# Performance work log

Measured on AMD Instinct MI355X. Metric: run time of the kernel, lower is better.

## Reference

```python
import jax, jax.numpy as jnp
import numpy as np

N = 50000   # nodes
E = 100000  # directed edges
G = 2048    # graphs in batch
D = 32      # hidden dim
F_NODE = 11
F_EDGE = 4


def setup_inputs() -> dict:
    key = jax.random.key(0)
    ks = jax.random.split(key, 12)
    s = 0.1
    return {
        "x": jax.random.normal(ks[0], (N, F_NODE), dtype=jnp.float32),
        "edge_attr": jax.random.uniform(ks[1], (E, F_EDGE), dtype=jnp.float32),
        "lin0_w": jax.random.normal(ks[2], (D, F_NODE), dtype=jnp.float32) * s,
        "lin0_b": jnp.zeros((D,), jnp.float32),
        "nn_w": jax.random.normal(ks[3], (D * D, F_EDGE), dtype=jnp.float32) * s,
        "nn_b": jnp.zeros((D * D,), jnp.float32),
        "root_w": jax.random.normal(ks[4], (D, D), dtype=jnp.float32) * s,
        "conv_b": jnp.zeros((D,), jnp.float32),
        "gru_wi": jax.random.normal(ks[5], (3 * D, D), dtype=jnp.float32) * s,
        "gru_wh": jax.random.normal(ks[6], (3 * D, D), dtype=jnp.float32) * s,
        "gru_bi": jnp.zeros((3 * D,), jnp.float32),
        "gru_bh": jnp.zeros((3 * D,), jnp.float32),
        "lin1_w": jax.random.normal(ks[7], (2, D), dtype=jnp.float32) * s,
        "lin1_b": jnp.zeros((2,), jnp.float32),
        "edge_index": jax.random.randint(ks[8], (2, E), 0, N, dtype=jnp.int32),
        "batch": jnp.sort(jax.random.randint(ks[9], (N,), 0, G, dtype=jnp.int32)),
    }


def _gru_step(m, h, wi, wh, bi, bh):
    # single-step torch.nn.GRU cell math
    gi = m @ wi.T + bi            # [N, 3D]
    gh = h @ wh.T + bh            # [N, 3D]
    ir, iz, inn = jnp.split(gi, 3, axis=-1)
    hr, hz, hn = jnp.split(gh, 3, axis=-1)
    r = jax.nn.sigmoid(ir + hr)
    z = jax.nn.sigmoid(iz + hz)
    n = jnp.tanh(inn + r * hn)
    return (1.0 - z) * n + z * h


def reference(x, edge_attr, lin0_w, lin0_b, nn_w, nn_b, root_w, conv_b,
              gru_wi, gru_wh, gru_bi, gru_bh, lin1_w, lin1_b,
              edge_index, batch):
    src, dst = edge_index[0], edge_index[1]
    out = jax.nn.relu(x @ lin0_w.T + lin0_b)   # [N, D]
    h = out
    # per-edge 32x32 weight from edge MLP (edge_attr fixed -> hoisted out of loop)
    W_e = (edge_attr @ nn_w.T + nn_b).reshape(E, D, D)
    for _ in range(3):
        msg = jnp.einsum('ei,eio->eo', out[src], W_e)                  # [E, D]
        aggr = jax.ops.segment_sum(msg, dst, num_segments=N)           # add-aggregate
        m = jax.nn.relu(aggr + out @ root_w + conv_b)                  # NNConv root + bias
        h = _gru_step(m, h, gru_wi, gru_wh, gru_bi, gru_bh)
        out = h
    cnt = jax.ops.segment_sum(jnp.ones((N,), x.dtype), batch, num_segments=G)
    pooled = jax.ops.segment_sum(out, batch, num_segments=G) / jnp.maximum(cnt, 1.0)[:, None]
    logits = pooled @ lin1_w.T + lin1_b                                # [G, 2]
    return jax.nn.log_softmax(logits, axis=1)
```

## Files before the change

kernel.cpp:

```cpp
#include <hip/hip_runtime.h>
#include <hip/hip_bf16.h>

#define NN 50000
#define EE 100000
#define GG 2048
#define NB2 391

__device__ __forceinline__ float b2f(unsigned short u) {
    union { unsigned int i; float f; } x; x.i = (unsigned int)u << 16; return x.f;
}
__device__ __forceinline__ unsigned short f2b(float f) {
    union { float f; unsigned int i; } x; x.f = f;
    unsigned int b = x.i + (0x7FFFu + ((x.i >> 16) & 1u));
    return (unsigned short)(b >> 16);
}

__global__ void k_init(const float* __restrict__ x, const float* __restrict__ w,
                       const float* __restrict__ b, float* __restrict__ feat) {
    int idx = blockIdx.x * blockDim.x + threadIdx.x;
    if (idx >= NN * 32) return;
    int n = idx >> 5, o = idx & 31;
    const float* xr = x + n * 11;
    const float* wr = w + o * 11;
    float acc = b[o];
#pragma unroll
    for (int i = 0; i < 11; ++i) acc += xr[i] * wr[i];
    feat[idx] = fmaxf(acc, 0.f);
}

__global__ void k_prep(const float* __restrict__ nnw, const float* __restrict__ nnb,
                       const float* __restrict__ wi, const float* __restrict__ wh,
                       float* __restrict__ Wre, float* __restrict__ WyT,
                       float* __restrict__ wiT, float* __restrict__ whT) {
    int idx = blockIdx.x * blockDim.x + threadIdx.x;
    if (idx < 5120) {
        int c = idx >> 5, i = idx & 31;
        float v;
        if (c < 128) v = nnw[((i << 5) + (c & 31)) * 4 + (c >> 5)];
        else         v = nnb[(i << 5) + (c - 128)];
        Wre[idx] = v;
    } else if (idx < 10240) {
        int j = idx - 5120;
        int i = j / 160, c = j - i * 160;
        float v;
        if (c < 128) v = nnw[((i << 5) + (c & 31)) * 4 + (c >> 5)];
        else         v = nnb[(i << 5) + (c - 128)];
        WyT[j] = v;
    } else if (idx < 13312) {
        int j = idx - 10240;
        int k = j / 96, c = j - k * 96;
        wiT[j] = wi[c * 32 + k];
    } else if (idx < 16384) {
        int j = idx - 13312;
        int k = j / 96, c = j - k * 96;
        whT[j] = wh[c * 32 + k];
    }
}

__global__ void k_hist(const int* __restrict__ ei, int* __restrict__ cnt) {
    int e = blockIdx.x * blockDim.x + threadIdx.x;
    if (e >= EE) return;
    atomicAdd(&cnt[ei[EE + e]], 1);
    atomicAdd(&cnt[NN + ei[e]], 1);
}

__global__ __launch_bounds__(256) void k_scan1(const int* __restrict__ cnt,
                                               int* __restrict__ tmp,
                                               int* __restrict__ bsum) {
    __shared__ int sd[256];
    int t = threadIdx.x;
    int i = blockIdx.x * 256 + t;
    int v = (i < 2 * NN) ? cnt[i] : 0;
    sd[t] = v;
    __syncthreads();
#pragma unroll
    for (int off = 1; off < 256; off <<= 1) {
        int x = (t >= off) ? sd[t - off] : 0;
        __syncthreads();
        sd[t] += x;
        __syncthreads();
    }
    if (i < 2 * NN) tmp[i] = sd[t];
    if (t == 255) bsum[blockIdx.x] = sd[255];
}

__global__ __launch_bounds__(512) void k_scan2(int* __restrict__ bsum) {
    __shared__ int sd[512];
    int t = threadIdx.x;
    int v = (t < NB2) ? bsum[t] : 0;
    sd[t] = v;
    __syncthreads();
#pragma unroll
    for (int off = 1; off < 512; off <<= 1) {
        int x = (t >= off) ? sd[t - off] : 0;
        __syncthreads();
        sd[t] += x;
        __syncthreads();
    }
    if (t < NB2) bsum[t] = sd[t];
}

__global__ void k_scan3(const int* __restrict__ cnt, const int* __restrict__ tmp,
                        const int* __restrict__ bsum, int* __restrict__ row_ptr,
                        int* __restrict__ cursor, int* __restrict__ out_ptr,
                        int* __restrict__ cursor2) {
    int i = blockIdx.x * blockDim.x + threadIdx.x;
    if (i >= 2 * NN) return;
    int base = (blockIdx.x > 0) ? bsum[blockIdx.x - 1] : 0;
    int excl = base + tmp[i] - cnt[i];
    if (i < NN) {
        row_ptr[i] = excl;
        cursor[i] = excl;
        if (i == 0) row_ptr[NN] = EE;
    } else {
        int j = i - NN;
        out_ptr[j] = excl - EE;
        cursor2[j] = excl - EE;
        if (j == 0) out_ptr[NN] = EE;
    }
}

__global__ void k_scatter(const int* __restrict__ ei, const float* __restrict__ ea,
                          int* __restrict__ cursor, int* __restrict__ cursor2,
                          int* __restrict__ esrc, float4* __restrict__ eea,
                          int* __restrict__ oslot, float4* __restrict__ oea) {
    int e = blockIdx.x * blockDim.x + threadIdx.x;
    if (e >= EE) return;
    int s = ei[e], d = ei[EE + e];
    float4 a = make_float4(ea[e * 4 + 0], ea[e * 4 + 1], ea[e * 4 + 2], ea[e * 4 + 3]);
    int slot = atomicAdd(&cursor[d], 1);
    esrc[slot] = s;
    eea[slot] = a;
    int pos = atomicAdd(&cursor2[s], 1);
    oslot[pos] = slot;
    oea[pos] = a;
}

__global__ __launch_bounds__(256) void k_y(const float* __restrict__ feat,
                                           const float* __restrict__ Wre,
                                           unsigned short* __restrict__ yb) {
    int lane = threadIdx.x & 63;
    int wv = __builtin_amdgcn_readfirstlane(threadIdx.x >> 6);
    int n = blockIdx.x * 64 + lane;
    if (n >= NN) return;
    int c0 = blockIdx.y * 40 + wv * 10;
    float fr[32];
    const float4* f4 = (const float4*)(feat + (long)n * 32);
#pragma unroll
    for (int q = 0; q < 8; ++q) {
        float4 v = f4[q];
        fr[4 * q + 0] = v.x; fr[4 * q + 1] = v.y;
        fr[4 * q + 2] = v.z; fr[4 * q + 3] = v.w;
    }
    float acc[10];
#pragma unroll
    for (int cc = 0; cc < 10; ++cc) {
        const float* w = Wre + (c0 + cc) * 32;
        float a = 0.f;
#pragma unroll
        for (int i = 0; i < 32; ++i) a += fr[i] * w[i];
        acc[cc] = a;
    }
    unsigned short* yr = yb + (long)n * 160 + c0;
#pragma unroll
    for (int q = 0; q < 5; ++q) {
        unsigned int wlo = f2b(acc[2 * q]);
        unsigned int whi = f2b(acc[2 * q + 1]);
        ((unsigned int*)yr)[q] = wlo | (whi << 16);
    }
}

__global__ __launch_bounds__(256) void k_msg(
    const unsigned short* __restrict__ yb, const int* __restrict__ esrc,
    const float4* __restrict__ eea, float* __restrict__ msg) {
    int idx = blockIdx.x * 256 + threadIdx.x;
    if (idx >= EE * 32) return;
    int slot = idx >> 5, o = idx & 31;
    int s = esrc[slot];
    float4 a = eea[slot];
    const unsigned short* yr = yb + (long)s * 160;
    float y0 = b2f(yr[o]);
    float y1 = b2f(yr[32 + o]);
    float y2 = b2f(yr[64 + o]);
    float y3 = b2f(yr[96 + o]);
    float y4 = b2f(yr[128 + o]);
    msg[idx] = y4 + a.x * y0 + a.y * y1 + a.z * y2 + a.w * y3;
}

__global__ __launch_bounds__(256) void k_conv_update(
    const float* __restrict__ msg_in, const int* __restrict__ row_ptr,
    const float* __restrict__ rootw, const float* __restrict__ convb,
    const float* __restrict__ wiT, const float* __restrict__ whT,
    const float* __restrict__ bi, const float* __restrict__ bh,
    const float* __restrict__ WyT, const int* __restrict__ out_ptr,
    const int* __restrict__ oslot, const float4* __restrict__ oea,
    float* __restrict__ feat, float* __restrict__ msg_out, int write_msg) {
    __shared__ float fs[32][32];
    __shared__ float ms[32][32];
    int t = threadIdx.x;
    int g = t >> 5, o = t & 31;
    int nb = blockIdx.x * 32 + g * 4;
    float f[4], m[4];
#pragma unroll
    for (int j = 0; j < 4; ++j) {
        int n = nb + j;
        bool v = (n < NN);
        f[j] = v ? feat[(long)n * 32 + o] : 0.f;
        fs[g * 4 + j][o] = f[j];
        m[j] = convb[o];
        if (v) {
            int e0 = row_ptr[n], e1 = row_ptr[n + 1];
            for (int e = e0; e < e1; ++e)
                m[j] += msg_in[((long)e << 5) + o];
        }
    }
    __syncthreads();
#pragma unroll 4
    for (int i = 0; i < 32; ++i) {
        float rw = rootw[i * 32 + o];
#pragma unroll
        for (int j = 0; j < 4; ++j) m[j] += fs[g * 4 + j][i] * rw;
    }
#pragma unroll
    for (int j = 0; j < 4; ++j) {
        m[j] = fmaxf(m[j], 0.f);
        ms[g * 4 + j][o] = m[j];
    }
    __syncthreads();
    float bir = bi[o], biz = bi[32 + o], bin_ = bi[64 + o];
    float bhr = bh[o], bhz = bh[32 + o], bhn = bh[64 + o];
    float gir[4], giz[4], gin_[4], ghr[4], ghz[4], ghn[4];
#pragma unroll
    for (int j = 0; j < 4; ++j) {
        gir[j] = bir; giz[j] = biz; gin_[j] = bin_;
        ghr[j] = bhr; ghz[j] = bhz; ghn[j] = bhn;
    }
#pragma unroll 2
    for (int k = 0; k < 32; ++k) {
        const float* wik = wiT + k * 96 + o;
        const float* whk = whT + k * 96 + o;
        float wir = wik[0], wiz = wik[32], win = wik[64];
        float whr = whk[0], whz = whk[32], whn = whk[64];
#pragma unroll
        for (int j = 0; j < 4; ++j) {
            float mk = ms[g * 4 + j][k], hk = fs[g * 4 + j][k];
            gir[j] += mk * wir;
            giz[j] += mk * wiz;
            gin_[j] += mk * win;
            ghr[j] += hk * whr;
            ghz[j] += hk * whz;
            ghn[j] += hk * whn;
        }
    }
    float fn[4];
#pragma unroll
    for (int j = 0; j < 4; ++j) {
        int n = nb + j;
        float r = 1.f / (1.f + __expf(-(gir[j] + ghr[j])));
        float z = 1.f / (1.f + __expf(-(giz[j] + ghz[j])));
        float nt = tanhf(gin_[j] + r * ghn[j]);
        fn[j] = (1.f - z) * nt + z * f[j];
        if (n < NN) feat[(long)n * 32 + o] = fn[j];
    }
    if (!write_msg) return;
#pragma unroll
    for (int j = 0; j < 4; ++j) fs[g * 4 + j][o] = fn[j];
    float ya[4][5];
#pragma unroll
    for (int j = 0; j < 4; ++j)
#pragma unroll
        for (int q = 0; q < 5; ++q) ya[j][q] = 0.f;
#pragma unroll 4
    for (int i = 0; i < 32; ++i) {
        const float* wy = WyT + i * 160 + o;
        float w0 = wy[0], w1 = wy[32], w2 = wy[64], w3 = wy[96], w4 = wy[128];
#pragma unroll
        for (int j = 0; j < 4; ++j) {
            float fv = fs[g * 4 + j][i];
            ya[j][0] += fv * w0;
            ya[j][1] += fv * w1;
            ya[j][2] += fv * w2;
            ya[j][3] += fv * w3;
            ya[j][4] += fv * w4;
        }
    }
#pragma unroll
    for (int j = 0; j < 4; ++j) {
        int n = nb + j;
        if (n < NN) {
            int p0 = out_ptr[n], p1 = out_ptr[n + 1];
            for (int p = p0; p < p1; ++p) {
                float4 a = oea[p];
                int slot = oslot[p];
                msg_out[((long)slot << 5) + o] =
                    ya[j][4] + a.x * ya[j][0] + a.y * ya[j][1]
                             + a.z * ya[j][2] + a.w * ya[j][3];
            }
        }
    }
}

__global__ __launch_bounds__(64) void k_pool_final(
    const float* __restrict__ feat, const int* __restrict__ batch,
    const float* __restrict__ w, const float* __restrict__ b,
    float* __restrict__ out) {
    int g = blockIdx.x;
    int t = threadIdx.x;
    int o = t & 31, h = t >> 5;
    int lo = 0, hi = NN;
    while (lo < hi) { int mid = (lo + hi) >> 1; if (batch[mid] < g) lo = mid + 1; else hi = mid; }
    int start = lo;
    hi = NN;
    while (lo < hi) { int mid = (lo + hi) >> 1; if (batch[mid] <= g) lo = mid + 1; else hi = mid; }
    int end = lo;
    float acc = 0.f;
    for (int n = start + h; n < end; n += 2) acc += feat[(long)n * 32 + o];
    acc += __shfl_xor(acc, 32, 64);
    float p = acc / fmaxf((float)(end - start), 1.f);
    float l0 = p * w[o], l1 = p * w[32 + o];
#pragma unroll
    for (int s = 16; s >= 1; s >>= 1) {
        l0 += __shfl_xor(l0, s, 64);
        l1 += __shfl_xor(l1, s, 64);
    }
    if (t == 0) {
        l0 += b[0]; l1 += b[1];
        float mx = fmaxf(l0, l1);
        float lse = mx + logf(__expf(l0 - mx) + __expf(l1 - mx));
        out[g * 2 + 0] = l0 - lse;
        out[g * 2 + 1] = l1 - lse;
    }
}

extern "C" void kernel_launch(void* const* d_in, const int* in_sizes, int n_in,
                              void* d_out, int out_size, void* d_ws, size_t ws_size,
                              hipStream_t stream) {
    const float* x        = (const float*)d_in[0];
    const float* edge_attr= (const float*)d_in[1];
    const float* lin0_w   = (const float*)d_in[2];
    const float* lin0_b   = (const float*)d_in[3];
    const float* nn_w     = (const float*)d_in[4];
    const float* nn_b     = (const float*)d_in[5];
    const float* root_w   = (const float*)d_in[6];
    const float* conv_b   = (const float*)d_in[7];
    const float* gru_wi   = (const float*)d_in[8];
    const float* gru_wh   = (const float*)d_in[9];
    const float* gru_bi   = (const float*)d_in[10];
    const float* gru_bh   = (const float*)d_in[11];
    const float* lin1_w   = (const float*)d_in[12];
    const float* lin1_b   = (const float*)d_in[13];
    const int*   edge_idx = (const int*)d_in[14];
    const int*   batch    = (const int*)d_in[15];
    float* out = (float*)d_out;

    float* ws     = (float*)d_ws;
    float* feat   = ws;
    float* Wre    = feat + (long)NN * 32;
    float* WyT    = Wre + 5120;
    float* wiT    = WyT + 5120;
    float* whT    = wiT + 3072;
    int*   cnt    = (int*)(whT + 3072);
    int*   tmp    = cnt + 2 * NN;
    int*   bsum   = tmp + 2 * NN;
    int*   row_ptr= bsum + 512;
    int*   cursor = row_ptr + NN + 1;
    int*   out_ptr= cursor + NN;
    int*   cursor2= out_ptr + NN + 1;
    int*   esrc   = cursor2 + NN;
    int*   oslot  = esrc + EE;
    size_t off = ((size_t)((char*)(oslot + EE) - (char*)d_ws) + 15) & ~(size_t)15;
    float4* eea  = (float4*)((char*)d_ws + off);
    float4* oea  = eea + EE;
    unsigned short* yb = (unsigned short*)(oea + EE);
    float* msgA  = (float*)(yb + (long)NN * 160);
    float* msgB  = msgA + (long)EE * 32;

    hipMemsetAsync(cnt, 0, 2 * NN * sizeof(int), stream);

    k_prep<<<64, 256, 0, stream>>>(nn_w, nn_b, gru_wi, gru_wh, Wre, WyT, wiT, whT);
    k_init<<<(NN * 32 + 255) / 256, 256, 0, stream>>>(x, lin0_w, lin0_b, feat);

    k_hist<<<(EE + 255) / 256, 256, 0, stream>>>(edge_idx, cnt);
    k_scan1<<<NB2, 256, 0, stream>>>(cnt, tmp, bsum);
    k_scan2<<<1, 512, 0, stream>>>(bsum);
    k_scan3<<<NB2, 256, 0, stream>>>(cnt, tmp, bsum, row_ptr, cursor, out_ptr, cursor2);
    k_scatter<<<(EE + 255) / 256, 256, 0, stream>>>(edge_idx, edge_attr, cursor, cursor2,
                                                    esrc, eea, oslot, oea);

    dim3 gy((NN + 63) / 64, 4);
    k_y<<<gy, 256, 0, stream>>>(feat, Wre, yb);
    k_msg<<<(EE * 32 + 255) / 256, 256, 0, stream>>>(yb, esrc, eea, msgA);

    k_conv_update<<<(NN + 31) / 32, 256, 0, stream>>>(msgA, row_ptr, root_w, conv_b,
                                                      wiT, whT, gru_bi, gru_bh, WyT,
                                                      out_ptr, oslot, oea,
                                                      feat, msgB, 1);
    k_conv_update<<<(NN + 31) / 32, 256, 0, stream>>>(msgB, row_ptr, root_w, conv_b,
                                                      wiT, whT, gru_bi, gru_bh, WyT,
                                                      out_ptr, oslot, oea,
                                                      feat, msgA, 1);
    k_conv_update<<<(NN + 31) / 32, 256, 0, stream>>>(msgA, row_ptr, root_w, conv_b,
                                                      wiT, whT, gru_bi, gru_bh, WyT,
                                                      out_ptr, oslot, oea,
                                                      feat, msgB, 0);

    k_pool_final<<<GG, 64, 0, stream>>>(feat, batch, lin1_w, lin1_b, out);
}
```

Measured before the change: 293.0 us.

## Merge setup kernels, fuse scatter with y, pack conv weights into float4 with packed FMA

Combines the init, prep and histogram kernels into one launch, and the scatter and y-projection kernels into another, to cut launch count and gaps. In the conv/GRU update kernel, the root and hidden-GRU weights are packed into one float4 table and the input-GRU weights into another. The root and hidden-gate matmuls now share one loop, shared memory is transposed and padded for float4 reads, and the arithmetic uses two-wide packed FMAs. The message projection now reads nn_w directly as float4, which removes the WyT transpose. The risks are higher register pressure and branch-divergent block roles inside the merged kernels.

```diff
diff --git a/kernel.cpp b/kernel.cpp
--- a/kernel.cpp
+++ b/kernel.cpp
@@ -6,6 +6,11 @@
 #define GG 2048
 #define NB2 391
 
+typedef float v2f __attribute__((ext_vector_type(2)));
+__device__ __forceinline__ v2f fma2(v2f a, float b, v2f c) {
+    return __builtin_elementwise_fma(a, (v2f){b, b}, c);
+}
+
 __device__ __forceinline__ float b2f(unsigned short u) {
     union { unsigned int i; float f; } x; x.i = (unsigned int)u << 16; return x.f;
 }
@@ -15,53 +20,51 @@
     return (unsigned short)(b >> 16);
 }
 
-__global__ void k_init(const float* __restrict__ x, const float* __restrict__ w,
-                       const float* __restrict__ b, float* __restrict__ feat) {
-    int idx = blockIdx.x * blockDim.x + threadIdx.x;
-    if (idx >= NN * 32) return;
-    int n = idx >> 5, o = idx & 31;
-    const float* xr = x + n * 11;
-    const float* wr = w + o * 11;
-    float acc = b[o];
-#pragma unroll
-    for (int i = 0; i < 11; ++i) acc += xr[i] * wr[i];
-    feat[idx] = fmaxf(acc, 0.f);
-}
-
-__global__ void k_prep(const float* __restrict__ nnw, const float* __restrict__ nnb,
-                       const float* __restrict__ wi, const float* __restrict__ wh,
-                       float* __restrict__ Wre, float* __restrict__ WyT,
-                       float* __restrict__ wiT, float* __restrict__ whT) {
-    int idx = blockIdx.x * blockDim.x + threadIdx.x;
-    if (idx < 5120) {
-        int c = idx >> 5, i = idx & 31;
-        float v;
-        if (c < 128) v = nnw[((i << 5) + (c & 31)) * 4 + (c >> 5)];
-        else         v = nnb[(i << 5) + (c - 128)];
-        Wre[idx] = v;
-    } else if (idx < 10240) {
-        int j = idx - 5120;
-        int i = j / 160, c = j - i * 160;
-        float v;
-        if (c < 128) v = nnw[((i << 5) + (c & 31)) * 4 + (c >> 5)];
-        else         v = nnb[(i << 5) + (c - 128)];
-        WyT[j] = v;
-    } else if (idx < 13312) {
-        int j = idx - 10240;
-        int k = j / 96, c = j - k * 96;
-        wiT[j] = wi[c * 32 + k];
-    } else if (idx < 16384) {
-        int j = idx - 13312;
-        int k = j / 96, c = j - k * 96;
-        whT[j] = wh[c * 32 + k];
-    }
-}
-
-__global__ void k_hist(const int* __restrict__ ei, int* __restrict__ cnt) {
-    int e = blockIdx.x * blockDim.x + threadIdx.x;
-    if (e >= EE) return;
-    atomicAdd(&cnt[ei[EE + e]], 1);
-    atomicAdd(&cnt[NN + ei[e]], 1);
+__global__ __launch_bounds__(256) void k_setup(
+    const float* __restrict__ x, const float* __restrict__ lw,
+    const float* __restrict__ lb, const float* __restrict__ nnw,
+    const float* __restrict__ nnb, const float* __restrict__ rootw,
+    const float* __restrict__ wi, const float* __restrict__ wh,
+    const int* __restrict__ ei, float* __restrict__ feat,
+    float* __restrict__ Wre, float4* __restrict__ rw4,
+    float4* __restrict__ wi4, int* __restrict__ cnt) {
+    int blk = blockIdx.x;
+    int t = threadIdx.x;
+    if (blk < 6250) {
+        int idx = blk * 256 + t;
+        if (idx >= NN * 32) return;
+        int n = idx >> 5, o = idx & 31;
+        const float* xr = x + n * 11;
+        const float* wr = lw + o * 11;
+        float acc = lb[o];
+#pragma unroll
+        for (int i = 0; i < 11; ++i) acc += xr[i] * wr[i];
+        feat[idx] = fmaxf(acc, 0.f);
+    } else if (blk < 6278) {
+        int idx = (blk - 6250) * 256 + t;
+        if (idx < 5120) {
+            int c = idx >> 5, i = idx & 31;
+            float v;
+            if (c < 128) v = nnw[((i << 5) + (c & 31)) * 4 + (c >> 5)];
+            else         v = nnb[(i << 5) + (c - 128)];
+            Wre[idx] = v;
+        } else if (idx < 6144) {
+            int j = idx - 5120;
+            int k = j >> 5, o = j & 31;
+            rw4[j] = make_float4(rootw[k * 32 + o], wh[o * 32 + k],
+                                 wh[(32 + o) * 32 + k], wh[(64 + o) * 32 + k]);
+        } else if (idx < 7168) {
+            int j = idx - 6144;
+            int k = j >> 5, o = j & 31;
+            wi4[j] = make_float4(wi[o * 32 + k], wi[(32 + o) * 32 + k],
+                                 wi[(64 + o) * 32 + k], 0.f);
+        }
+    } else {
+        int e = (blk - 6278) * 256 + t;
+        if (e >= EE) return;
+        atomicAdd(&cnt[ei[EE + e]], 1);
+        atomicAdd(&cnt[NN + ei[e]], 1);
+    }
 }
 
 __global__ __launch_bounds__(256) void k_scan1(const int* __restrict__ cnt,
@@ -120,37 +123,41 @@
     }
 }
 
-__global__ void k_scatter(const int* __restrict__ ei, const float* __restrict__ ea,
-                          int* __restrict__ cursor, int* __restrict__ cursor2,
-                          int* __restrict__ esrc, float4* __restrict__ eea,
-                          int* __restrict__ oslot, float4* __restrict__ oea) {
-    int e = blockIdx.x * blockDim.x + threadIdx.x;
-    if (e >= EE) return;
-    int s = ei[e], d = ei[EE + e];
-    float4 a = make_float4(ea[e * 4 + 0], ea[e * 4 + 1], ea[e * 4 + 2], ea[e * 4 + 3]);
-    int slot = atomicAdd(&cursor[d], 1);
-    esrc[slot] = s;
-    eea[slot] = a;
-    int pos = atomicAdd(&cursor2[s], 1);
-    oslot[pos] = slot;
-    oea[pos] = a;
-}
-
-__global__ __launch_bounds__(256) void k_y(const float* __restrict__ feat,
-                                           const float* __restrict__ Wre,
-                                           unsigned short* __restrict__ yb) {
+__global__ __launch_bounds__(256) void k_scatter_y(
+    const int* __restrict__ ei, const float* __restrict__ ea,
+    int* __restrict__ cursor, int* __restrict__ cursor2,
+    int* __restrict__ esrc, float4* __restrict__ eea,
+    int* __restrict__ oslot, float4* __restrict__ oea,
+    const float* __restrict__ feat, const float* __restrict__ Wre,
+    unsigned short* __restrict__ yb) {
+    int blk = blockIdx.x;
+    if (blk < 391) {
+        int e = blk * 256 + threadIdx.x;
+        if (e >= EE) return;
+        int s = ei[e], d = ei[EE + e];
+        float4 a = make_float4(ea[e * 4 + 0], ea[e * 4 + 1], ea[e * 4 + 2], ea[e * 4 + 3]);
+        int slot = atomicAdd(&cursor[d], 1);
+        esrc[slot] = s;
+        eea[slot] = a;
+        int pos = atomicAdd(&cursor2[s], 1);
+        oslot[pos] = slot;
+        oea[pos] = a;
+        return;
+    }
+    int by = blk - 391;
+    int bx = by % 782, q = by / 782;
     int lane = threadIdx.x & 63;
     int wv = __builtin_amdgcn_readfirstlane(threadIdx.x >> 6);
-    int n = blockIdx.x * 64 + lane;
+    int n = bx * 64 + lane;
     if (n >= NN) return;
-    int c0 = blockIdx.y * 40 + wv * 10;
+    int c0 = q * 40 + wv * 10;
     float fr[32];
     const float4* f4 = (const float4*)(feat + (long)n * 32);
 #pragma unroll
-    for (int q = 0; q < 8; ++q) {
-        float4 v = f4[q];
-        fr[4 * q + 0] = v.x; fr[4 * q + 1] = v.y;
-        fr[4 * q + 2] = v.z; fr[4 * q + 3] = v.w;
+    for (int qq = 0; qq < 8; ++qq) {
+        float4 v = f4[qq];
+        fr[4 * qq + 0] = v.x; fr[4 * qq + 1] = v.y;
+        fr[4 * qq + 2] = v.z; fr[4 * qq + 3] = v.w;
     }
     float acc[10];
 #pragma unroll
@@ -163,10 +170,10 @@
     }
     unsigned short* yr = yb + (long)n * 160 + c0;
 #pragma unroll
-    for (int q = 0; q < 5; ++q) {
-        unsigned int wlo = f2b(acc[2 * q]);
-        unsigned int whi = f2b(acc[2 * q + 1]);
-        ((unsigned int*)yr)[q] = wlo | (whi << 16);
+    for (int qq = 0; qq < 5; ++qq) {
+        unsigned int wlo = f2b(acc[2 * qq]);
+        unsigned int whi = f2b(acc[2 * qq + 1]);
+        ((unsigned int*)yr)[qq] = wlo | (whi << 16);
     }
 }
 
@@ -189,101 +196,109 @@
 
 __global__ __launch_bounds__(256) void k_conv_update(
     const float* __restrict__ msg_in, const int* __restrict__ row_ptr,
-    const float* __restrict__ rootw, const float* __restrict__ convb,
-    const float* __restrict__ wiT, const float* __restrict__ whT,
-    const float* __restrict__ bi, const float* __restrict__ bh,
-    const float* __restrict__ WyT, const int* __restrict__ out_ptr,
+    const float4* __restrict__ rw4, const float* __restrict__ convb,
+    const float4* __restrict__ wi4, const float* __restrict__ bi,
+    const float* __restrict__ bh, const float4* __restrict__ nnw4,
+    const float* __restrict__ nnb, const int* __restrict__ out_ptr,
     const int* __restrict__ oslot, const float4* __restrict__ oea,
     float* __restrict__ feat, float* __restrict__ msg_out, int write_msg) {
-    __shared__ float fs[32][32];
-    __shared__ float ms[32][32];
+    __shared__ float fsT[32][36];
+    __shared__ float msT[32][36];
     int t = threadIdx.x;
     int g = t >> 5, o = t & 31;
-    int nb = blockIdx.x * 32 + g * 4;
+    int gc = g * 4;
+    int nb = blockIdx.x * 32 + gc;
     float f[4], m[4];
+    float cb = convb[o];
 #pragma unroll
     for (int j = 0; j < 4; ++j) {
         int n = nb + j;
         bool v = (n < NN);
-        f[j] = v ? feat[(long)n * 32 + o] : 0.f;
-        fs[g * 4 + j][o] = f[j];
-        m[j] = convb[o];
+        f[j] = v ? feat[n * 32 + o] : 0.f;
+        m[j] = cb;
         if (v) {
             int e0 = row_ptr[n], e1 = row_ptr[n + 1];
             for (int e = e0; e < e1; ++e)
-                m[j] += msg_in[((long)e << 5) + o];
+                m[j] += msg_in[(e << 5) + o];
         }
     }
+    *(float4*)&fsT[o][gc] = make_float4(f[0], f[1], f[2], f[3]);
     __syncthreads();
+
+    float bhr = bh[o], bhz = bh[32 + o], bhn = bh[64 + o];
+    v2f m01 = {m[0], m[1]}, m23 = {m[2], m[3]};
+    v2f ghr01 = {bhr, bhr}, ghr23 = {bhr, bhr};
+    v2f ghz01 = {bhz, bhz}, ghz23 = {bhz, bhz};
+    v2f ghn01 = {bhn, bhn}, ghn23 = {bhn, bhn};
 #pragma unroll 4
     for (int i = 0; i < 32; ++i) {
-        float rw = rootw[i * 32 + o];
-#pragma unroll
-        for (int j = 0; j < 4; ++j) m[j] += fs[g * 4 + j][i] * rw;
-    }
-#pragma unroll
-    for (int j = 0; j < 4; ++j) {
-        m[j] = fmaxf(m[j], 0.f);
-        ms[g * 4 + j][o] = m[j];
-    }
+        float4 w = rw4[i * 32 + o];
+        float4 fv = *(const float4*)&fsT[i][gc];
+        v2f f01 = {fv.x, fv.y}, f23 = {fv.z, fv.w};
+        m01 = fma2(f01, w.x, m01);   m23 = fma2(f23, w.x, m23);
+        ghr01 = fma2(f01, w.y, ghr01); ghr23 = fma2(f23, w.y, ghr23);
+        ghz01 = fma2(f01, w.z, ghz01); ghz23 = fma2(f23, w.z, ghz23);
+        ghn01 = fma2(f01, w.w, ghn01); ghn23 = fma2(f23, w.w, ghn23);
+    }
+    float mm0 = fmaxf(m01.x, 0.f), mm1 = fmaxf(m01.y, 0.f);
+    float mm2 = fmaxf(m23.x, 0.f), mm3 = fmaxf(m23.y, 0.f);
+    *(float4*)&msT[o][gc] = make_float4(mm0, mm1, mm2, mm3);
     __syncthreads();
+
     float bir = bi[o], biz = bi[32 + o], bin_ = bi[64 + o];
-    float bhr = bh[o], bhz = bh[32 + o], bhn = bh[64 + o];
-    float gir[4], giz[4], gin_[4], ghr[4], ghz[4], ghn[4];
-#pragma unroll
-    for (int j = 0; j < 4; ++j) {
-        gir[j] = bir; giz[j] = biz; gin_[j] = bin_;
-        ghr[j] = bhr; ghz[j] = bhz; ghn[j] = bhn;
-    }
-#pragma unroll 2
+    v2f gir01 = {bir, bir}, gir23 = {bir, bir};
+    v2f giz01 = {biz, biz}, giz23 = {biz, biz};
+    v2f gin01 = {bin_, bin_}, gin23 = {bin_, bin_};
+#pragma unroll 4
     for (int k = 0; k < 32; ++k) {
-        const float* wik = wiT + k * 96 + o;
-        const float* whk = whT + k * 96 + o;
-        float wir = wik[0], wiz = wik[32], win = wik[64];
-        float whr = whk[0], whz = whk[32], whn = whk[64];
-#pragma unroll
-        for (int j = 0; j < 4; ++j) {
-            float mk = ms[g * 4 + j][k], hk = fs[g * 4 + j][k];
-            gir[j] += mk * wir;
-            giz[j] += mk * wiz;
-            gin_[j] += mk * win;
-            ghr[j] += hk * whr;
-            ghz[j] += hk * whz;
-            ghn[j] += hk * whn;
-        }
-    }
+        float4 w = wi4[k * 32 + o];
+        float4 mv = *(const float4*)&msT[k][gc];
+        v2f p01 = {mv.x, mv.y}, p23 = {mv.z, mv.w};
+        gir01 = fma2(p01, w.x, gir01); gir23 = fma2(p23, w.x, gir23);
+        giz01 = fma2(p01, w.y, giz01); giz23 = fma2(p23, w.y, giz23);
+        gin01 = fma2(p01, w.z, gin01); gin23 = fma2(p23, w.z, gin23);
+    }
+    float girA[4] = {gir01.x, gir01.y, gir23.x, gir23.y};
+    float gizA[4] = {giz01.x, giz01.y, giz23.x, giz23.y};
+    float ginA[4] = {gin01.x, gin01.y, gin23.x, gin23.y};
+    float ghrA[4] = {ghr01.x, ghr01.y, ghr23.x, ghr23.y};
+    float ghzA[4] = {ghz01.x, ghz01.y, ghz23.x, ghz23.y};
+    float ghnA[4] = {ghn01.x, ghn01.y, ghn23.x, ghn23.y};
     float fn[4];
 #pragma unroll
     for (int j = 0; j < 4; ++j) {
         int n = nb + j;
-        float r = 1.f / (1.f + __expf(-(gir[j] + ghr[j])));
-        float z = 1.f / (1.f + __expf(-(giz[j] + ghz[j])));
-        float nt = tanhf(gin_[j] + r * ghn[j]);
+        float r = 1.f / (1.f + __expf(-(girA[j] + ghrA[j])));
+        float z = 1.f / (1.f + __expf(-(gizA[j] + ghzA[j])));
+        float nt = tanhf(ginA[j] + r * ghnA[j]);
         fn[j] = (1.f - z) * nt + z * f[j];
-        if (n < NN) feat[(long)n * 32 + o] = fn[j];
+        if (n < NN) feat[n * 32 + o] = fn[j];
     }
     if (!write_msg) return;
-#pragma unroll
-    for (int j = 0; j < 4; ++j) fs[g * 4 + j][o] = fn[j];
-    float ya[4][5];
-#pragma unroll
-    for (int j = 0; j < 4; ++j)
-#pragma unroll
-        for (int q = 0; q < 5; ++q) ya[j][q] = 0.f;
+
+    *(float4*)&fsT[o][gc] = make_float4(fn[0], fn[1], fn[2], fn[3]);
+    v2f y0_01 = {0.f, 0.f}, y0_23 = {0.f, 0.f};
+    v2f y1_01 = {0.f, 0.f}, y1_23 = {0.f, 0.f};
+    v2f y2_01 = {0.f, 0.f}, y2_23 = {0.f, 0.f};
+    v2f y3_01 = {0.f, 0.f}, y3_23 = {0.f, 0.f};
+    v2f y4_01 = {0.f, 0.f}, y4_23 = {0.f, 0.f};
 #pragma unroll 4
     for (int i = 0; i < 32; ++i) {
-        const float* wy = WyT + i * 160 + o;
-        float w0 = wy[0], w1 = wy[32], w2 = wy[64], w3 = wy[96], w4 = wy[128];
-#pragma unroll
-        for (int j = 0; j < 4; ++j) {
-            float fv = fs[g * 4 + j][i];
-            ya[j][0] += fv * w0;
-            ya[j][1] += fv * w1;
-            ya[j][2] += fv * w2;
-            ya[j][3] += fv * w3;
-            ya[j][4] += fv * w4;
-        }
-    }
+        float4 w = nnw4[i * 32 + o];
+        float w1 = nnb[i * 32 + o];
+        float4 fv = *(const float4*)&fsT[i][gc];
+        v2f f01 = {fv.x, fv.y}, f23 = {fv.z, fv.w};
+        y0_01 = fma2(f01, w.x, y0_01); y0_23 = fma2(f23, w.x, y0_23);
+        y1_01 = fma2(f01, w.y, y1_01); y1_23 = fma2(f23, w.y, y1_23);
+        y2_01 = fma2(f01, w.z, y2_01); y2_23 = fma2(f23, w.z, y2_23);
+        y3_01 = fma2(f01, w.w, y3_01); y3_23 = fma2(f23, w.w, y3_23);
+        y4_01 = fma2(f01, w1, y4_01);  y4_23 = fma2(f23, w1, y4_23);
+    }
+    float ya0[4] = {y0_01.x, y0_01.y, y0_23.x, y0_23.y};
+    float ya1[4] = {y1_01.x, y1_01.y, y1_23.x, y1_23.y};
+    float ya2[4] = {y2_01.x, y2_01.y, y2_23.x, y2_23.y};
+    float ya3[4] = {y3_01.x, y3_01.y, y3_23.x, y3_23.y};
+    float ya4[4] = {y4_01.x, y4_01.y, y4_23.x, y4_23.y};
 #pragma unroll
     for (int j = 0; j < 4; ++j) {
         int n = nb + j;
@@ -292,9 +307,9 @@
             for (int p = p0; p < p1; ++p) {
                 float4 a = oea[p];
                 int slot = oslot[p];
-                msg_out[((long)slot << 5) + o] =
-                    ya[j][4] + a.x * ya[j][0] + a.y * ya[j][1]
-                             + a.z * ya[j][2] + a.w * ya[j][3];
+                msg_out[(slot << 5) + o] =
+                    ya4[j] + a.x * ya0[j] + a.y * ya1[j]
+                           + a.z * ya2[j] + a.w * ya3[j];
             }
         }
     }
@@ -353,54 +368,50 @@
     const int*   batch    = (const int*)d_in[15];
     float* out = (float*)d_out;
 
-    float* ws     = (float*)d_ws;
-    float* feat   = ws;
-    float* Wre    = feat + (long)NN * 32;
-    float* WyT    = Wre + 5120;
-    float* wiT    = WyT + 5120;
-    float* whT    = wiT + 3072;
-    int*   cnt    = (int*)(whT + 3072);
-    int*   tmp    = cnt + 2 * NN;
-    int*   bsum   = tmp + 2 * NN;
-    int*   row_ptr= bsum + 512;
-    int*   cursor = row_ptr + NN + 1;
-    int*   out_ptr= cursor + NN;
-    int*   cursor2= out_ptr + NN + 1;
-    int*   esrc   = cursor2 + NN;
-    int*   oslot  = esrc + EE;
-    size_t off = ((size_t)((char*)(oslot + EE) - (char*)d_ws) + 15) & ~(size_t)15;
-    float4* eea  = (float4*)((char*)d_ws + off);
-    float4* oea  = eea + EE;
-    unsigned short* yb = (unsigned short*)(oea + EE);
-    float* msgA  = (float*)(yb + (long)NN * 160);
-    float* msgB  = msgA + (long)EE * 32;
+    float4* rw4   = (float4*)d_ws;
+    float4* wi4   = rw4 + 1024;
+    float4* eea   = wi4 + 1024;
+    float4* oea   = eea + EE;
+    float*  feat  = (float*)(oea + EE);
+    float*  Wre   = feat + (long)NN * 32;
+    int*    cnt   = (int*)(Wre + 5120);
+    int*    tmp   = cnt + 2 * NN;
+    int*    bsum  = tmp + 2 * NN;
+    int*    row_ptr = bsum + 512;
+    int*    cursor  = row_ptr + NN + 1;
+    int*    out_ptr = cursor + NN;
+    int*    cursor2 = out_ptr + NN + 1;
+    int*    esrc  = cursor2 + NN;
+    int*    oslot = esrc + EE;
+    unsigned short* yb = (unsigned short*)(oslot + EE);
+    float*  msgA  = (float*)(yb + (long)NN * 160);
+    float*  msgB  = msgA + (long)EE * 32;
+    const float4* nnw4 = (const float4*)nn_w;
 
     hipMemsetAsync(cnt, 0, 2 * NN * sizeof(int), stream);
 
-    k_prep<<<64, 256, 0, stream>>>(nn_w, nn_b, gru_wi, gru_wh, Wre, WyT, wiT, whT);
-    k_init<<<(NN * 32 + 255) / 256, 256, 0, stream>>>(x, lin0_w, lin0_b, feat);
-
-    k_hist<<<(EE + 255) / 256, 256, 0, stream>>>(edge_idx, cnt);
+    k_setup<<<6250 + 28 + 391, 256, 0, stream>>>(x, lin0_w, lin0_b, nn_w, nn_b,
+                                                 root_w, gru_wi, gru_wh, edge_idx,
+                                                 feat, Wre, rw4, wi4, cnt);
+
     k_scan1<<<NB2, 256, 0, stream>>>(cnt, tmp, bsum);
     k_scan2<<<1, 512, 0, stream>>>(bsum);
     k_scan3<<<NB2, 256, 0, stream>>>(cnt, tmp, bsum, row_ptr, cursor, out_ptr, cursor2);
-    k_scatter<<<(EE + 255) / 256, 256, 0, stream>>>(edge_idx, edge_attr, cursor, cursor2,
-                                                    esrc, eea, oslot, oea);
-
-    dim3 gy((NN + 63) / 64, 4);
-    k_y<<<gy, 256, 0, stream>>>(feat, Wre, yb);
+
+    k_scatter_y<<<391 + 782 * 4, 256, 0, stream>>>(edge_idx, edge_attr, cursor, cursor2,
+                                                   esrc, eea, oslot, oea, feat, Wre, yb);
     k_msg<<<(EE * 32 + 255) / 256, 256, 0, stream>>>(yb, esrc, eea, msgA);
 
-    k_conv_update<<<(NN + 31) / 32, 256, 0, stream>>>(msgA, row_ptr, root_w, conv_b,
-                                                      wiT, whT, gru_bi, gru_bh, WyT,
+    k_conv_update<<<(NN + 31) / 32, 256, 0, stream>>>(msgA, row_ptr, rw4, conv_b, wi4,
+                                                      gru_bi, gru_bh, nnw4, nn_b,
                                                       out_ptr, oslot, oea,
                                                       feat, msgB, 1);
-    k_conv_update<<<(NN + 31) / 32, 256, 0, stream>>>(msgB, row_ptr, root_w, conv_b,
-                                                      wiT, whT, gru_bi, gru_bh, WyT,
+    k_conv_update<<<(NN + 31) / 32, 256, 0, stream>>>(msgB, row_ptr, rw4, conv_b, wi4,
+                                                      gru_bi, gru_bh, nnw4, nn_b,
                                                       out_ptr, oslot, oea,
                                                       feat, msgA, 1);
-    k_conv_update<<<(NN + 31) / 32, 256, 0, stream>>>(msgA, row_ptr, root_w, conv_b,
-                                                      wiT, whT, gru_bi, gru_bh, WyT,
+    k_conv_update<<<(NN + 31) / 32, 256, 0, stream>>>(msgA, row_ptr, rw4, conv_b, wi4,
+                                                      gru_bi, gru_bh, nnw4, nn_b,
                                                       out_ptr, oslot, oea,
                                                       feat, msgB, 0);
 
```

Result: faster. 273.4 us (-6.7%).
